# Kernel tuning notes

Hardware: AMD Instinct MI355X
Metric: run time of the kernel (lower is better)

The kernel has to match this reference:

```python
import jax, jax.numpy as jnp
import numpy as np

ALPHA = 0.2  # LeakyReLU negative slope
NEG_INF = -9e15


def setup_inputs() -> dict:
    key = jax.random.key(0)
    k1, k2, k3, k4 = jax.random.split(key, 4)
    N, F_IN, F_OUT = 8192, 128, 64
    h = jax.random.normal(k1, (N, F_IN), dtype=jnp.float32)
    adj = jax.random.randint(k2, (N, N), 0, 2, dtype=jnp.int32)
    # xavier_uniform with gain=1.414 (as in the torch module)
    gain = 1.414
    bW = gain * np.sqrt(6.0 / (F_IN + F_OUT))
    W = jax.random.uniform(k3, (F_IN, F_OUT), dtype=jnp.float32, minval=-bW, maxval=bW)
    ba = gain * np.sqrt(6.0 / (2 * F_OUT + 1))
    a = jax.random.uniform(k4, (2 * F_OUT, 1), dtype=jnp.float32, minval=-ba, maxval=ba)
    return {"h": h, "adj": adj, "W": W, "a": a}


def reference(h, adj, W, a):
    # Wh: [N, F_out]
    Wh = h @ W
    F_out = Wh.shape[1]
    # Decompose a^T [Wh_i || Wh_j] = (Wh @ a_src)_i + (Wh @ a_dst)_j
    # (same math as the repeat+concat construction, without the N*N*2F tensor)
    src = Wh @ a[:F_out, 0]   # [N]
    dst = Wh @ a[F_out:, 0]   # [N]
    e = jax.nn.leaky_relu(src[:, None] + dst[None, :], negative_slope=ALPHA)  # [N, N]
    e = jnp.where(adj > 0, e, jnp.float32(NEG_INF))
    attention = jax.nn.softmax(e, axis=1)  # [N, N]
    h_prime = attention @ Wh               # [N, F_out]
    return jax.nn.elu(h_prime)
```

## Files before the change

kernel.cpp:

```cpp
#include <hip/hip_runtime.h>

#define ALPHA 0.2f
#define NN 8192
#define FIN 128
#define FOUT 64

typedef short bf16x8 __attribute__((ext_vector_type(8)));
typedef float f32x4 __attribute__((ext_vector_type(4)));

__device__ __forceinline__ unsigned short f2b(float x) {
    unsigned u = __builtin_bit_cast(unsigned, x);
    unsigned r = (u + 0x7fffu + ((u >> 16) & 1u)) >> 16;
    return (unsigned short)r;
}

__global__ __launch_bounds__(256) void gat_k1(const float* __restrict__ h,
                                              const float* __restrict__ W,
                                              const float* __restrict__ a,
                                              float* __restrict__ Wh,
                                              float* __restrict__ src,
                                              float* __restrict__ dst) {
    __shared__ float wlds[FIN * FOUT];
    int t = threadIdx.x;
    const float4* W4 = (const float4*)W;
    float4* wlds4 = (float4*)wlds;
#pragma unroll
    for (int q = 0; q < 8; ++q) wlds4[q * 256 + t] = W4[q * 256 + t];
    __syncthreads();
    int wave = t >> 6, lane = t & 63;
    int row = blockIdx.x * 4 + wave;
    const float4* h4 = (const float4*)(h + (size_t)row * FIN);
    float acc = 0.f;
#pragma unroll
    for (int k4 = 0; k4 < 32; ++k4) {
        float4 hv = h4[k4];
        acc = fmaf(hv.x, wlds[(k4 * 4 + 0) * 64 + lane], acc);
        acc = fmaf(hv.y, wlds[(k4 * 4 + 1) * 64 + lane], acc);
        acc = fmaf(hv.z, wlds[(k4 * 4 + 2) * 64 + lane], acc);
        acc = fmaf(hv.w, wlds[(k4 * 4 + 3) * 64 + lane], acc);
    }
    Wh[(size_t)row * 64 + lane] = acc;
    float sa = acc * a[lane];
    float da = acc * a[64 + lane];
#pragma unroll
    for (int off = 32; off; off >>= 1) {
        sa += __shfl_xor(sa, off);
        da += __shfl_xor(da, off);
    }
    if (lane == 0) { src[row] = sa; dst[row] = da; }
}

__global__ __launch_bounds__(256) void gat_k1b(const float* __restrict__ Wh,
                                               unsigned short* __restrict__ whbt) {
    __shared__ unsigned short t16[64 * 68];
    int t = threadIdx.x;
    int rb = blockIdx.x * 64;
    const float4* s4 = (const float4*)(Wh + (size_t)rb * 64);
#pragma unroll
    for (int q = 0; q < 4; ++q) {
        float4 v = s4[t * 4 + q];
        int flat = t * 16 + q * 4;
        int r = flat >> 6, f = flat & 63;
        unsigned short* p = &t16[r * 68 + f];
        p[0] = f2b(v.x); p[1] = f2b(v.y); p[2] = f2b(v.z); p[3] = f2b(v.w);
    }
    __syncthreads();
    int f = t >> 2, qr = t & 3;
    unsigned v[8];
#pragma unroll
    for (int k = 0; k < 8; ++k) {
        unsigned lo = t16[(qr * 16 + 2 * k + 0) * 68 + f];
        unsigned hi = t16[(qr * 16 + 2 * k + 1) * 68 + f];
        v[k] = lo | (hi << 16);
    }
    uint4* o = (uint4*)(whbt + (size_t)f * NN + rb + qr * 16);
    o[0] = make_uint4(v[0], v[1], v[2], v[3]);
    o[1] = make_uint4(v[4], v[5], v[6], v[7]);
}

__global__ __launch_bounds__(256) void gat_k2(const int* __restrict__ adj,
                                              const unsigned short* __restrict__ whbt,
                                              const float* __restrict__ src,
                                              const float* __restrict__ dst,
                                              float* __restrict__ pl,
                                              float* __restrict__ pacc,
                                              int ns, int js) {
    const int l = threadIdx.x & 63;
    const int w = threadIdx.x >> 6;
    const int r = l & 15;
    const int g = l >> 4;
    const int s = blockIdx.x;
    const int rg = blockIdx.y;
    const int task = rg * ns + s;
    const int rowbase = rg * 64 + w * 16;
    const int row = rowbase + r;
    const int j0 = s * js, jend = j0 + js;

    const float srcv = src[row];
    const int4* adjrow4 = (const int4*)(adj + (size_t)row * NN);
    const float4* dst4 = (const float4*)dst;

    f32x4 acc0 = {0.f, 0.f, 0.f, 0.f}, acc1 = acc0, acc2 = acc0, acc3 = acc0;
    float lsum = 0.f;

    int4 ca0 = adjrow4[(j0 >> 2) + 2 * g];
    int4 ca1 = adjrow4[(j0 >> 2) + 2 * g + 1];

    for (int jc = j0; jc < jend; jc += 32) {
        int nx = jc + 32;
        int4 na0, na1;
        if (nx < jend) {
            na0 = adjrow4[(nx >> 2) + 2 * g];
            na1 = adjrow4[(nx >> 2) + 2 * g + 1];
        }
        float4 d0 = dst4[(jc >> 2) + 2 * g];
        float4 d1 = dst4[(jc >> 2) + 2 * g + 1];

        float p[8];
        {
            float xs[8] = {d0.x, d0.y, d0.z, d0.w, d1.x, d1.y, d1.z, d1.w};
            int ms[8] = {ca0.x, ca0.y, ca0.z, ca0.w, ca1.x, ca1.y, ca1.z, ca1.w};
#pragma unroll
            for (int e = 0; e < 8; ++e) {
                float x = srcv + xs[e];
                float lr = x > 0.f ? x : ALPHA * x;
                float pe = (ms[e] != 0) ? __expf(lr) : 0.f;
                p[e] = pe;
                lsum += pe;
            }
        }
        bf16x8 af;
#pragma unroll
        for (int e = 0; e < 8; ++e) af[e] = (short)f2b(p[e]);

        const unsigned short* bbase = whbt + (size_t)r * NN + jc + 8 * g;
        bf16x8 b0 = *(const bf16x8*)(bbase + 0 * 16 * NN);
        bf16x8 b1 = *(const bf16x8*)(bbase + 1 * 16 * NN);
        bf16x8 b2 = *(const bf16x8*)(bbase + 2 * 16 * NN);
        bf16x8 b3 = *(const bf16x8*)(bbase + 3 * 16 * NN);
        acc0 = __builtin_amdgcn_mfma_f32_16x16x32_bf16(af, b0, acc0, 0, 0, 0);
        acc1 = __builtin_amdgcn_mfma_f32_16x16x32_bf16(af, b1, acc1, 0, 0, 0);
        acc2 = __builtin_amdgcn_mfma_f32_16x16x32_bf16(af, b2, acc2, 0, 0, 0);
        acc3 = __builtin_amdgcn_mfma_f32_16x16x32_bf16(af, b3, acc3, 0, 0, 0);

        ca0 = na0; ca1 = na1;
    }

    lsum += __shfl_xor(lsum, 16);
    lsum += __shfl_xor(lsum, 32);
    if (l < 16) pl[(size_t)task * 64 + w * 16 + l] = lsum;

    float* po = pacc + (size_t)task * 4096 + (size_t)(w * 16) * 64;
#pragma unroll
    for (int reg = 0; reg < 4; ++reg) {
        int m = g * 4 + reg;
        po[m * 64 + 0 * 16 + r] = acc0[reg];
        po[m * 64 + 1 * 16 + r] = acc1[reg];
        po[m * 64 + 2 * 16 + r] = acc2[reg];
        po[m * 64 + 3 * 16 + r] = acc3[reg];
    }
}

__global__ __launch_bounds__(256) void gat_k3(const float* __restrict__ pl,
                                              const float* __restrict__ pacc,
                                              float* __restrict__ out, int ns) {
    int t = threadIdx.x;
    int wave = t >> 6, lane = t & 63;
    int row = blockIdx.x * 4 + wave;
    int rg = row >> 6, rr = row & 63;
    float L = 0.f, o = 0.f;
    for (int s2 = 0; s2 < ns; ++s2) {
        L += pl[(size_t)(rg * ns + s2) * 64 + rr];
        o += pacc[(size_t)(rg * ns + s2) * 4096 + rr * 64 + lane];
    }
    float hp = o / L;
    out[(size_t)row * 64 + lane] = hp > 0.f ? hp : __expf(hp) - 1.f;
}

extern "C" void kernel_launch(void* const* d_in, const int* in_sizes, int n_in,
                              void* d_out, int out_size, void* d_ws, size_t ws_size,
                              hipStream_t stream) {
    const float* h = (const float*)d_in[0];
    const int* adj = (const int*)d_in[1];
    const float* W = (const float*)d_in[2];
    const float* a = (const float*)d_in[3];
    float* out = (float*)d_out;
    float* ws = (float*)d_ws;

    size_t avail = ws_size / sizeof(float);
    int ns = 8;
    while (ns > 1 && (size_t)802816 + (size_t)ns * 532480 > avail) ns >>= 1;
    int js = NN / ns;

    float* Wh = ws;
    float* src = Wh + (size_t)NN * FOUT;
    float* dst = src + NN;
    float* pl = dst + NN;
    float* pacc = pl + (size_t)128 * ns * 64;
    unsigned short* whbt = (unsigned short*)(pacc + (size_t)128 * ns * 4096);

    gat_k1<<<dim3(NN / 4), dim3(256), 0, stream>>>(h, W, a, Wh, src, dst);
    gat_k1b<<<dim3(NN / 64), dim3(256), 0, stream>>>(Wh, whbt);
    gat_k2<<<dim3(ns, 128), dim3(256), 0, stream>>>(adj, whbt, src, dst, pl, pacc, ns, js);
    gat_k3<<<dim3(NN / 4), dim3(256), 0, stream>>>(pl, pacc, out, ns);
}
```

Baseline: 429.5 us.

## Deepen adj prefetch, compute row sums via MFMA with ones, use packed bf16 convert

```diff
diff --git a/kernel.cpp b/kernel.cpp
--- a/kernel.cpp
+++ b/kernel.cpp
@@ -92,63 +92,70 @@
     const int s = blockIdx.x;
     const int rg = blockIdx.y;
     const int task = rg * ns + s;
-    const int rowbase = rg * 64 + w * 16;
-    const int row = rowbase + r;
+    const int row = rg * 64 + w * 16 + r;
     const int j0 = s * js, jend = j0 + js;
 
     const float srcv = src[row];
-    const int4* adjrow4 = (const int4*)(adj + (size_t)row * NN);
+    const int4* adjr = (const int4*)(adj + (size_t)row * NN);
     const float4* dst4 = (const float4*)dst;
 
-    f32x4 acc0 = {0.f, 0.f, 0.f, 0.f}, acc1 = acc0, acc2 = acc0, acc3 = acc0;
-    float lsum = 0.f;
-
-    int4 ca0 = adjrow4[(j0 >> 2) + 2 * g];
-    int4 ca1 = adjrow4[(j0 >> 2) + 2 * g + 1];
-
-    for (int jc = j0; jc < jend; jc += 32) {
-        int nx = jc + 32;
-        int4 na0, na1;
-        if (nx < jend) {
-            na0 = adjrow4[(nx >> 2) + 2 * g];
-            na1 = adjrow4[(nx >> 2) + 2 * g + 1];
-        }
-        float4 d0 = dst4[(jc >> 2) + 2 * g];
-        float4 d1 = dst4[(jc >> 2) + 2 * g + 1];
-
-        float p[8];
-        {
+    f32x4 acc0 = {0.f, 0.f, 0.f, 0.f}, acc1 = acc0, acc2 = acc0, acc3 = acc0, accl = acc0;
+    bf16x8 bones;
+#pragma unroll
+    for (int e = 0; e < 8; ++e) bones[e] = (short)0x3F80;
+
+    int base = (j0 >> 2) + 2 * g;
+    int4 c0 = adjr[base], c1 = adjr[base + 1], c2 = adjr[base + 8], c3 = adjr[base + 9];
+
+    for (int jc = j0; jc < jend; jc += 64) {
+        int nj = jc + 64;
+        int pj = (nj < jend) ? nj : j0;
+        int nb = (pj >> 2) + 2 * g;
+        int4 n0 = adjr[nb], n1 = adjr[nb + 1], n2 = adjr[nb + 8], n3 = adjr[nb + 9];
+
+#pragma unroll
+        for (int half = 0; half < 2; ++half) {
+            const int jh = jc + half * 32;
+            int4 ca = half ? c2 : c0;
+            int4 cb = half ? c3 : c1;
+            float4 d0 = dst4[(jh >> 2) + 2 * g];
+            float4 d1 = dst4[(jh >> 2) + 2 * g + 1];
             float xs[8] = {d0.x, d0.y, d0.z, d0.w, d1.x, d1.y, d1.z, d1.w};
-            int ms[8] = {ca0.x, ca0.y, ca0.z, ca0.w, ca1.x, ca1.y, ca1.z, ca1.w};
+            int ms[8] = {ca.x, ca.y, ca.z, ca.w, cb.x, cb.y, cb.z, cb.w};
+            float p[8];
 #pragma unroll
             for (int e = 0; e < 8; ++e) {
                 float x = srcv + xs[e];
-                float lr = x > 0.f ? x : ALPHA * x;
-                float pe = (ms[e] != 0) ? __expf(lr) : 0.f;
-                p[e] = pe;
-                lsum += pe;
+                float lr = fmaxf(x, 0.f) + ALPHA * fminf(x, 0.f);
+                float pe = __expf(lr);
+                p[e] = (ms[e] != 0) ? pe : 0.f;
             }
+            unsigned pw0, pw1, pw2, pw3;
+            asm("v_cvt_pk_bf16_f32 %0, %1, %2" : "=v"(pw0) : "v"(p[0]), "v"(p[1]));
+            asm("v_cvt_pk_bf16_f32 %0, %1, %2" : "=v"(pw1) : "v"(p[2]), "v"(p[3]));
+            asm("v_cvt_pk_bf16_f32 %0, %1, %2" : "=v"(pw2) : "v"(p[4]), "v"(p[5]));
+            asm("v_cvt_pk_bf16_f32 %0, %1, %2" : "=v"(pw3) : "v"(p[6]), "v"(p[7]));
+            uint4 pwv = make_uint4(pw0, pw1, pw2, pw3);
+            bf16x8 af = __builtin_bit_cast(bf16x8, pwv);
+
+            const unsigned short* bbase = whbt + (size_t)r * NN + jh + 8 * g;
+            bf16x8 b0 = *(const bf16x8*)(bbase + 0 * 16 * NN);
+            bf16x8 b1 = *(const bf16x8*)(bbase + 1 * 16 * NN);
+            bf16x8 b2 = *(const bf16x8*)(bbase + 2 * 16 * NN);
+            bf16x8 b3 = *(const bf16x8*)(bbase + 3 * 16 * NN);
+            acc0 = __builtin_amdgcn_mfma_f32_16x16x32_bf16(af, b0, acc0, 0, 0, 0);
+            acc1 = __builtin_amdgcn_mfma_f32_16x16x32_bf16(af, b1, acc1, 0, 0, 0);
+            acc2 = __builtin_amdgcn_mfma_f32_16x16x32_bf16(af, b2, acc2, 0, 0, 0);
+            acc3 = __builtin_amdgcn_mfma_f32_16x16x32_bf16(af, b3, acc3, 0, 0, 0);
+            accl = __builtin_amdgcn_mfma_f32_16x16x32_bf16(af, bones, accl, 0, 0, 0);
         }
-        bf16x8 af;
-#pragma unroll
-        for (int e = 0; e < 8; ++e) af[e] = (short)f2b(p[e]);
-
-        const unsigned short* bbase = whbt + (size_t)r * NN + jc + 8 * g;
-        bf16x8 b0 = *(const bf16x8*)(bbase + 0 * 16 * NN);
-        bf16x8 b1 = *(const bf16x8*)(bbase + 1 * 16 * NN);
-        bf16x8 b2 = *(const bf16x8*)(bbase + 2 * 16 * NN);
-        bf16x8 b3 = *(const bf16x8*)(bbase + 3 * 16 * NN);
-        acc0 = __builtin_amdgcn_mfma_f32_16x16x32_bf16(af, b0, acc0, 0, 0, 0);
-        acc1 = __builtin_amdgcn_mfma_f32_16x16x32_bf16(af, b1, acc1, 0, 0, 0);
-        acc2 = __builtin_amdgcn_mfma_f32_16x16x32_bf16(af, b2, acc2, 0, 0, 0);
-        acc3 = __builtin_amdgcn_mfma_f32_16x16x32_bf16(af, b3, acc3, 0, 0, 0);
-
-        ca0 = na0; ca1 = na1;
-    }
-
-    lsum += __shfl_xor(lsum, 16);
-    lsum += __shfl_xor(lsum, 32);
-    if (l < 16) pl[(size_t)task * 64 + w * 16 + l] = lsum;
+        c0 = n0; c1 = n1; c2 = n2; c3 = n3;
+    }
+
+    if (r == 0) {
+        float* plo = pl + (size_t)task * 64 + w * 16 + g * 4;
+        plo[0] = accl[0]; plo[1] = accl[1]; plo[2] = accl[2]; plo[3] = accl[3];
+    }
 
     float* po = pacc + (size_t)task * 4096 + (size_t)(w * 16) * 64;
 #pragma unroll
```

Result: no change. 426.1 us (-0.8%).
